# Performance work log

Measured on AMD Instinct MI355X. Metric: run time of the kernel, lower is better.

Reference implementation:

```python
import jax, jax.numpy as jnp
import numpy as np

NEG = -1000.0  # matches the -1000 masking used in the original module


def setup_inputs() -> dict:
    key = jax.random.key(0)
    k0, k1, k2 = jax.random.split(key, 3)
    B, L, T = 512, 512, 32
    S = T + 2  # states: 0 = START, 1..T = tags, T+1 = STOP
    word_tag_value = jax.random.normal(k0, (B, L, T), dtype=jnp.float32)
    # xavier_uniform-style init for the transition matrix, then mask per the original
    a = float(np.sqrt(6.0 / (S + S)))
    translation = jax.random.uniform(k1, (S, S), dtype=jnp.float32, minval=-a, maxval=a)
    translation = translation.at[:, 0].set(NEG)       # nothing transitions into START
    translation = translation.at[S - 1, :].set(NEG)   # nothing transitions out of STOP
    real_tag = jax.random.randint(k2, (B, L), 1, T + 1)  # tags in 1..T
    return {"word_tag_value": word_tag_value, "translation": translation,
            "real_tag": real_tag, "output_loss": 1}


def _score_path(word_tag_value, translation, real_tag, T):
    # sum of emissions at the gold tags (tags 1..T index emission column tag-1)
    emit = jnp.take_along_axis(word_tag_value, (real_tag - 1)[..., None], axis=2)[..., 0]  # [B, L]
    score_emit = emit.sum(axis=1)
    # sum of transitions along the gold path + START/STOP transitions
    score_trans = translation[real_tag[:, :-1], real_tag[:, 1:]].sum(axis=1)
    score_trans = score_trans + translation[0, real_tag[:, 0]] + translation[real_tag[:, -1], T + 1]
    return score_emit + score_trans  # [B]


def _score_total(word_tag_value, translation, T):
    # forward algorithm (logsumexp recursion) over S = T+2 states
    B, L, _ = word_tag_value.shape
    # pad emissions to S states; START/STOP get NEG emission mid-sequence
    obs = jnp.pad(word_tag_value, ((0, 0), (0, 0), (1, 1)), constant_values=NEG)  # [B, L, S]
    # initial alpha: emissions of step 0 at tag states, 0 at START/STOP (as in original)
    alpha0 = jnp.pad(word_tag_value[:, 0, :], ((0, 0), (1, 1)), constant_values=0.0)  # [B, S]

    def step(alpha, obs_t):
        # scores[prev, cur] = alpha[prev] + obs_t[cur] + translation[prev, cur]
        m = alpha[:, :, None] + obs_t[:, None, :] + translation[None, :, :]  # [B, S, S]
        return jax.nn.logsumexp(m, axis=1), None

    alpha_T, _ = jax.lax.scan(step, alpha0, jnp.swapaxes(obs, 0, 1)[1:])  # scan over L-1 steps
    return jax.nn.logsumexp(alpha_T, axis=1)  # [B]


def reference(word_tag_value, translation, real_tag, output_loss):
    T = word_tag_value.shape[-1]
    if output_loss:
        return _score_total(word_tag_value, translation, T) - _score_path(word_tag_value, translation, real_tag, T)
    return None
```

## Files before the change

kernel.cpp:

```cpp
#include <hip/hip_runtime.h>


#define F2   1.4426950408889634f
#define LN2  0.6931471805599453f
#define BIAS 0.0078125f
#define BIASCNT 3577

__device__ __forceinline__ float grpmax32(float x) {
    int t;
    t = __builtin_amdgcn_update_dpp(__float_as_int(x), __float_as_int(x), 0x121, 0xf, 0xf, true);
    x = fmaxf(x, __int_as_float(t));
    t = __builtin_amdgcn_update_dpp(__float_as_int(x), __float_as_int(x), 0x122, 0xf, 0xf, true);
    x = fmaxf(x, __int_as_float(t));
    t = __builtin_amdgcn_update_dpp(__float_as_int(x), __float_as_int(x), 0x124, 0xf, 0xf, true);
    x = fmaxf(x, __int_as_float(t));
    t = __builtin_amdgcn_update_dpp(__float_as_int(x), __float_as_int(x), 0x128, 0xf, 0xf, true);
    x = fmaxf(x, __int_as_float(t));
    t = __builtin_amdgcn_ds_swizzle(__float_as_int(x), 0x401F);
    x = fmaxf(x, __int_as_float(t));
    return x;
}

__global__ __launch_bounds__(64) void crf_kernel(
    const float* __restrict__ wtv,
    const float* __restrict__ trans,
    const int*   __restrict__ rtag,
    float* __restrict__ out)
{
    __shared__ __align__(16) float tlds[1156];
    __shared__ __align__(16) int   ltag[1024];
    __shared__ __align__(16) float alds[160];

    const int l = threadIdx.x;
    const int q = l >> 5;
    const int c = l & 31;
    const int bbase = blockIdx.x * 2;

    for (int k = l; k < 1156; k += 64) tlds[k] = trans[k];
    {
        const int* rtb = rtag + (size_t)bbase * 512;
        for (int k = l; k < 1024; k += 64) ltag[k] = rtb[k];
    }
    __syncthreads();

    float tcF[32], tcB[32];
    #pragma unroll
    for (int k = 0; k < 32; ++k) {
        tcF[k] = __builtin_exp2f(F2 * tlds[(k + 1) * 34 + (c + 1)]) * BIAS;
        tcB[k] = __builtin_exp2f(F2 * tlds[(c + 1) * 34 + (k + 1)]) * BIAS;
    }
    float aiF = __builtin_exp2f(F2 * tlds[c + 1]) * BIAS;

    const float* wbq = wtv + (size_t)(bbase + q) * (512 * 32);

    float stF = __builtin_exp2f(F2 * wbq[c]);
    float stB = 1.0f;
    int scF = 0, scB = 0;

    float vnF[16], vnB[16];
    #pragma unroll
    for (int j = 0; j < 8; ++j) {
        vnF[j] = wbq[(1 + j) * 32 + c];
        vnB[j] = wbq[(511 - j) * 32 + c];
    }
    float eoF_c = __builtin_exp2f(F2 * vnF[0]);
    float gB    = stB * __builtin_exp2f(F2 * vnB[0]);

    float* aF = alds + q * 36;
    float* aB = alds + 80 + q * 36;
    const float4* f4 = (const float4*)aF;
    const float4* b4 = (const float4*)aB;

    float4 ra[8], rb[8];

    aF[c] = stF;
    __builtin_amdgcn_wave_barrier();
    #pragma unroll
    for (int k = 0; k < 8; ++k) ra[k] = f4[k];
    __builtin_amdgcn_wave_barrier();

    for (int t0 = 1; t0 <= 241; t0 += 16) {
        #pragma unroll
        for (int j = 0; j < 16; ++j) {
            const int i = t0 + j;

            aB[c] = gB;
            __builtin_amdgcn_wave_barrier();
            #pragma unroll
            for (int k = 0; k < 8; ++k) rb[k] = b4[k];
            __builtin_amdgcn_wave_barrier();
            vnB[(j + 8) & 15] = wbq[(512 - (i + 8)) * 32 + c];
            float eoB_n = __builtin_exp2f(F2 * vnB[(j + 1) & 15]);
            {
                float a0 = aiF, a1 = 0.0f, a2 = 0.0f, a3 = 0.0f;
                aiF = 0.0f;
                #pragma unroll
                for (int k = 0; k < 8; ++k) {
                    float4 x = ra[k];
                    a0 += x.x * tcF[4 * k + 0]; a1 += x.y * tcF[4 * k + 1];
                    a2 += x.z * tcF[4 * k + 2]; a3 += x.w * tcF[4 * k + 3];
                }
                float s = (a0 + a1) + (a2 + a3);
                stF = s * eoF_c;
            }
            if (j == 15) {
                float m = grpmax32(stF);
                int e = ((__float_as_int(m) >> 23) & 0xff) - 127;
                stF *= __int_as_float((127 - e) << 23);
                scF += e;
            }

            aF[c] = stF;
            __builtin_amdgcn_wave_barrier();
            #pragma unroll
            for (int k = 0; k < 8; ++k) ra[k] = f4[k];
            __builtin_amdgcn_wave_barrier();
            vnF[(j + 8) & 15] = wbq[(i + 8) * 32 + c];
            float eoF_n = __builtin_exp2f(F2 * vnF[(j + 1) & 15]);
            {
                float a0 = 0.0f, a1 = 0.0f, a2 = 0.0f, a3 = 0.0f;
                #pragma unroll
                for (int k = 0; k < 8; ++k) {
                    float4 x = rb[k];
                    a0 += x.x * tcB[4 * k + 0]; a1 += x.y * tcB[4 * k + 1];
                    a2 += x.z * tcB[4 * k + 2]; a3 += x.w * tcB[4 * k + 3];
                }
                float s = (a0 + a1) + (a2 + a3);
                if (j == 15) stB = (t0 != 241) ? s : stB;
                else         stB = s;
            }
            if (j == 15) {
                float m = grpmax32(stB);
                int e = ((__float_as_int(m) >> 23) & 0xff) - 127;
                stB *= __int_as_float((127 - e) << 23);
                scB += e;
            }
            gB   = stB * eoB_n;
            eoF_c = eoF_n;
        }
    }

    float prod = stF * stB;
    prod += __shfl_xor(prod, 1);
    prod += __shfl_xor(prod, 2);
    prod += __shfl_xor(prod, 4);
    prod += __shfl_xor(prod, 8);
    prod += __shfl_xor(prod, 16);
    float total = ((float)(scF + scB + BIASCNT) + __builtin_log2f(prod)) * LN2;

    float ps0 = 0.0f, ps1 = 0.0f;
    #pragma unroll
    for (int bb = 0; bb < 2; ++bb) {
        const float* w  = wtv + (size_t)(bbase + bb) * (512 * 32);
        const int*   tg = ltag + (bb << 9);
        int   tcur[8];
        float em[8];
        #pragma unroll
        for (int k = 0; k < 8; ++k) tcur[k] = tg[l + 64 * k];
        #pragma unroll
        for (int k = 0; k < 8; ++k) em[k] = w[(l + 64 * k) * 32 + (tcur[k] - 1)];
        float acc = 0.0f;
        #pragma unroll
        for (int k = 0; k < 8; ++k) {
            int t  = l + 64 * k;
            int nx = tg[(t + 1) & 511];
            nx = (t == 511) ? 33 : nx;
            acc += em[k] + tlds[tcur[k] * 34 + nx];
        }
        if (l == 0) acc += tlds[tg[0]];
        acc += __shfl_xor(acc, 1);
        acc += __shfl_xor(acc, 2);
        acc += __shfl_xor(acc, 4);
        acc += __shfl_xor(acc, 8);
        acc += __shfl_xor(acc, 16);
        acc += __shfl_xor(acc, 32);
        if (bb == 0) ps0 = acc; else ps1 = acc;
    }
    float ps = (q == 0) ? ps0 : ps1;
    if (c == 0) out[bbase + q] = total - ps;
}

extern "C" void kernel_launch(void* const* d_in, const int* in_sizes, int n_in,
                              void* d_out, int out_size, void* d_ws, size_t ws_size,
                              hipStream_t stream) {
    const float* wtv   = (const float*)d_in[0];
    const float* trans = (const float*)d_in[1];
    const int*   rtag  = (const int*)d_in[2];
    (void)in_sizes; (void)n_in; (void)d_ws; (void)ws_size; (void)out_size;
    float* out = (float*)d_out;
    crf_kernel<<<256, 64, 0, stream>>>(wtv, trans, rtag, out);
}
```

Before: 139.1 us.

## Split forward/backward recursions across half-waves with packed two-state FMA

Each 64-lane wave now runs the forward and backward CRF recursions at the same time. Each 16-lane quarter owns one direction for one batch element and handles two states per lane using f32x2 packed FMAs, so one step per iteration replaces the previous sequential forward-then-backward steps. The rescaling reduction shrinks to 16 lanes and runs once per 16-step block. This trades serial dependency length for more work per lane and more register pressure (launch_bounds with 1 block). The meet-in-the-middle combine now exchanges states across lanes.

New measurement: 146.8 us. 5.5% more time.

```diff
diff --git a/kernel.cpp b/kernel.cpp
--- a/kernel.cpp
+++ b/kernel.cpp
@@ -1,12 +1,14 @@
 #include <hip/hip_runtime.h>
 
+
+typedef float f32x2 __attribute__((ext_vector_type(2)));
 
 #define F2   1.4426950408889634f
 #define LN2  0.6931471805599453f
 #define BIAS 0.0078125f
 #define BIASCNT 3577
 
-__device__ __forceinline__ float grpmax32(float x) {
+__device__ __forceinline__ float grpmax16(float x) {
     int t;
     t = __builtin_amdgcn_update_dpp(__float_as_int(x), __float_as_int(x), 0x121, 0xf, 0xf, true);
     x = fmaxf(x, __int_as_float(t));
@@ -16,12 +18,10 @@
     x = fmaxf(x, __int_as_float(t));
     t = __builtin_amdgcn_update_dpp(__float_as_int(x), __float_as_int(x), 0x128, 0xf, 0xf, true);
     x = fmaxf(x, __int_as_float(t));
-    t = __builtin_amdgcn_ds_swizzle(__float_as_int(x), 0x401F);
-    x = fmaxf(x, __int_as_float(t));
     return x;
 }
 
-__global__ __launch_bounds__(64) void crf_kernel(
+__global__ __launch_bounds__(64, 1) void crf_kernel(
     const float* __restrict__ wtv,
     const float* __restrict__ trans,
     const int*   __restrict__ rtag,
@@ -29,11 +29,15 @@
 {
     __shared__ __align__(16) float tlds[1156];
     __shared__ __align__(16) int   ltag[1024];
-    __shared__ __align__(16) float alds[160];
+    __shared__ __align__(16) float alds[144];
 
-    const int l = threadIdx.x;
-    const int q = l >> 5;
-    const int c = l & 31;
+    const int l   = threadIdx.x;
+    const int q   = l >> 4;
+    const int c16 = l & 15;
+    const int h   = q & 1;
+    const int bp  = q >> 1;
+    const int sA  = 2 * c16;
+    const int sB  = sA + 1;
     const int bbase = blockIdx.x * 2;
 
     for (int k = l; k < 1156; k += 64) tlds[k] = trans[k];
@@ -43,110 +47,101 @@
     }
     __syncthreads();
 
-    float tcF[32], tcB[32];
+    f32x2 tc2[32];
     #pragma unroll
-    for (int k = 0; k < 32; ++k) {
-        tcF[k] = __builtin_exp2f(F2 * tlds[(k + 1) * 34 + (c + 1)]) * BIAS;
-        tcB[k] = __builtin_exp2f(F2 * tlds[(c + 1) * 34 + (k + 1)]) * BIAS;
+    for (int p = 0; p < 32; ++p) {
+        float tA = h ? tlds[(sA + 1) * 34 + (p + 1)] : tlds[(p + 1) * 34 + (sA + 1)];
+        float tB = h ? tlds[(sB + 1) * 34 + (p + 1)] : tlds[(p + 1) * 34 + (sB + 1)];
+        f32x2 v;
+        v.x = __builtin_exp2f(F2 * tA) * BIAS;
+        v.y = __builtin_exp2f(F2 * tB) * BIAS;
+        tc2[p] = v;
     }
-    float aiF = __builtin_exp2f(F2 * tlds[c + 1]) * BIAS;
+    f32x2 ai2 = {0.0f, 0.0f};
+    if (!h) {
+        ai2.x = __builtin_exp2f(F2 * tlds[sA + 1]) * BIAS;
+        ai2.y = __builtin_exp2f(F2 * tlds[sB + 1]) * BIAS;
+    }
 
-    const float* wbq = wtv + (size_t)(bbase + q) * (512 * 32);
+    const float* wbq = wtv + (size_t)(bbase + bp) * (512 * 32);
+    const float* wl  = wbq + sA;
 
-    float stF = __builtin_exp2f(F2 * wbq[c]);
-    float stB = 1.0f;
-    int scF = 0, scB = 0;
+    f32x2 st = {1.0f, 1.0f};
+    if (!h) {
+        f32x2 v0 = *(const f32x2*)wl;
+        st.x = __builtin_exp2f(F2 * v0.x);
+        st.y = __builtin_exp2f(F2 * v0.y);
+    }
+    int scaleE = 0;
 
-    float vnF[16], vnB[16];
+    f32x2 vn2[16];
     #pragma unroll
-    for (int j = 0; j < 8; ++j) {
-        vnF[j] = wbq[(1 + j) * 32 + c];
-        vnB[j] = wbq[(511 - j) * 32 + c];
-    }
-    float eoF_c = __builtin_exp2f(F2 * vnF[0]);
-    float gB    = stB * __builtin_exp2f(F2 * vnB[0]);
+    for (int j = 0; j < 8; ++j)
+        vn2[j] = *(const f32x2*)(wl + (h ? (511 - j) * 32 : (1 + j) * 32));
+    f32x2 eo_c;
+    eo_c.x = __builtin_exp2f(F2 * vn2[0].x);
+    eo_c.y = __builtin_exp2f(F2 * vn2[0].y);
 
-    float* aF = alds + q * 36;
-    float* aB = alds + 80 + q * 36;
-    const float4* f4 = (const float4*)aF;
-    const float4* b4 = (const float4*)aB;
+    float*        ach = alds + q * 36;
+    const float4* a4  = (const float4*)ach;
+    f32x2*        wp  = (f32x2*)(ach + sA);
 
-    float4 ra[8], rb[8];
-
-    aF[c] = stF;
-    __builtin_amdgcn_wave_barrier();
-    #pragma unroll
-    for (int k = 0; k < 8; ++k) ra[k] = f4[k];
-    __builtin_amdgcn_wave_barrier();
+    float4 ra[8];
 
     for (int t0 = 1; t0 <= 241; t0 += 16) {
         #pragma unroll
         for (int j = 0; j < 16; ++j) {
             const int i = t0 + j;
 
-            aB[c] = gB;
+            f32x2 wv = h ? st * eo_c : st;
+            *wp = wv;
             __builtin_amdgcn_wave_barrier();
             #pragma unroll
-            for (int k = 0; k < 8; ++k) rb[k] = b4[k];
+            for (int k = 0; k < 8; ++k) ra[k] = a4[k];
             __builtin_amdgcn_wave_barrier();
-            vnB[(j + 8) & 15] = wbq[(512 - (i + 8)) * 32 + c];
-            float eoB_n = __builtin_exp2f(F2 * vnB[(j + 1) & 15]);
-            {
-                float a0 = aiF, a1 = 0.0f, a2 = 0.0f, a3 = 0.0f;
-                aiF = 0.0f;
-                #pragma unroll
-                for (int k = 0; k < 8; ++k) {
-                    float4 x = ra[k];
-                    a0 += x.x * tcF[4 * k + 0]; a1 += x.y * tcF[4 * k + 1];
-                    a2 += x.z * tcF[4 * k + 2]; a3 += x.w * tcF[4 * k + 3];
-                }
-                float s = (a0 + a1) + (a2 + a3);
-                stF = s * eoF_c;
+            vn2[(j + 8) & 15] = *(const f32x2*)(wl + (h ? (512 - (i + 8)) * 32
+                                                       : (i + 8) * 32));
+            f32x2 vcn = vn2[(j + 1) & 15];
+            f32x2 eo_n;
+            eo_n.x = __builtin_exp2f(F2 * vcn.x);
+            eo_n.y = __builtin_exp2f(F2 * vcn.y);
+
+            f32x2 acc0 = ai2, acc1 = {0.0f, 0.0f};
+            f32x2 acc2 = {0.0f, 0.0f}, acc3 = {0.0f, 0.0f};
+            ai2.x = 0.0f; ai2.y = 0.0f;
+            #pragma unroll
+            for (int k = 0; k < 8; ++k) {
+                float4 x = ra[k];
+                f32x2 x0 = {x.x, x.x}, x1 = {x.y, x.y};
+                f32x2 x2 = {x.z, x.z}, x3 = {x.w, x.w};
+                acc0 = __builtin_elementwise_fma(x0, tc2[4 * k + 0], acc0);
+                acc1 = __builtin_elementwise_fma(x1, tc2[4 * k + 1], acc1);
+                acc2 = __builtin_elementwise_fma(x2, tc2[4 * k + 2], acc2);
+                acc3 = __builtin_elementwise_fma(x3, tc2[4 * k + 3], acc3);
             }
-            if (j == 15) {
-                float m = grpmax32(stF);
-                int e = ((__float_as_int(m) >> 23) & 0xff) - 127;
-                stF *= __int_as_float((127 - e) << 23);
-                scF += e;
-            }
+            f32x2 s2 = (acc0 + acc1) + (acc2 + acc3);
+            f32x2 ns = h ? s2 : s2 * eo_c;
 
-            aF[c] = stF;
-            __builtin_amdgcn_wave_barrier();
-            #pragma unroll
-            for (int k = 0; k < 8; ++k) ra[k] = f4[k];
-            __builtin_amdgcn_wave_barrier();
-            vnF[(j + 8) & 15] = wbq[(i + 8) * 32 + c];
-            float eoF_n = __builtin_exp2f(F2 * vnF[(j + 1) & 15]);
-            {
-                float a0 = 0.0f, a1 = 0.0f, a2 = 0.0f, a3 = 0.0f;
-                #pragma unroll
-                for (int k = 0; k < 8; ++k) {
-                    float4 x = rb[k];
-                    a0 += x.x * tcB[4 * k + 0]; a1 += x.y * tcB[4 * k + 1];
-                    a2 += x.z * tcB[4 * k + 2]; a3 += x.w * tcB[4 * k + 3];
-                }
-                float s = (a0 + a1) + (a2 + a3);
-                if (j == 15) stB = (t0 != 241) ? s : stB;
-                else         stB = s;
-            }
-            if (j == 15) {
-                float m = grpmax32(stB);
-                int e = ((__float_as_int(m) >> 23) & 0xff) - 127;
-                stB *= __int_as_float((127 - e) << 23);
-                scB += e;
-            }
-            gB   = stB * eoB_n;
-            eoF_c = eoF_n;
+            bool doUpd = (i != 256) || (h == 0);
+            st = doUpd ? ns : st;
+            eo_c = eo_n;
         }
+        float m = grpmax16(fmaxf(st.x, st.y));
+        int e = ((__float_as_int(m) >> 23) & 0xff) - 127;
+        float sc = __int_as_float((127 - e) << 23);
+        st.x *= sc; st.y *= sc;
+        scaleE += e;
     }
 
-    float prod = stF * stB;
+    float boA = __shfl_xor(st.x, 16);
+    float boB = __shfl_xor(st.y, 16);
+    float prod = st.x * boA + st.y * boB;
     prod += __shfl_xor(prod, 1);
     prod += __shfl_xor(prod, 2);
     prod += __shfl_xor(prod, 4);
     prod += __shfl_xor(prod, 8);
-    prod += __shfl_xor(prod, 16);
-    float total = ((float)(scF + scB + BIASCNT) + __builtin_log2f(prod)) * LN2;
+    int scTot = scaleE + __shfl_xor(scaleE, 16);
+    float total = ((float)(scTot + BIASCNT) + __builtin_log2f(prod)) * LN2;
 
     float ps0 = 0.0f, ps1 = 0.0f;
     #pragma unroll
@@ -176,8 +171,8 @@
         acc += __shfl_xor(acc, 32);
         if (bb == 0) ps0 = acc; else ps1 = acc;
     }
-    float ps = (q == 0) ? ps0 : ps1;
-    if (c == 0) out[bbase + q] = total - ps;
+    float ps = (bp == 0) ? ps0 : ps1;
+    if ((l & 31) == 0) out[bbase + bp] = total - ps;
 }
 
 extern "C" void kernel_launch(void* const* d_in, const int* in_sizes, int n_in,
```
